# Optimization experiments

Measured on AMD Instinct MI355X. Metric: run time of the kernel, lower is better.

Reference implementation:

```python
import jax, jax.numpy as jnp
import numpy as np

NQ = 4   # num qubits
NL = 2   # StronglyEntanglingLayers depth


def _apply_1q(state, U, w):
    # state: (B,2,2,2,2) complex64, U: (2,2) complex64, wire w in [0,NQ)
    state = jnp.moveaxis(state, w + 1, -1)
    state = jnp.einsum('ij,...j->...i', U, state)
    return jnp.moveaxis(state, -1, w + 1)


def _apply_cnot(state, cw, tw):
    # flip target axis on the control=1 slice
    s0 = jnp.take(state, jnp.array([0]), axis=cw + 1)
    s1 = jnp.take(state, jnp.array([1]), axis=cw + 1)
    s1 = jnp.flip(s1, axis=tw + 1)
    return jnp.concatenate([s0, s1], axis=cw + 1)


def _simulate(xq, qw):
    # xq: (B, NQ) angles/pi, qw: (NL, NQ, 3) Rot params
    half = 0.5 * jnp.pi * xq                      # RY(pi*x) half-angles
    c, s = jnp.cos(half), jnp.sin(half)           # (B, NQ)
    # RY on |0> gives [cos(t/2), sin(t/2)]: build product state directly
    state = jnp.stack([c[:, 0], s[:, 0]], axis=-1).astype(jnp.complex64)  # (B,2)
    for w in range(1, NQ):
        q = jnp.stack([c[:, w], s[:, w]], axis=-1).astype(jnp.complex64)
        state = jnp.einsum('b...,bj->b...j', state, q)  # -> (B,2,...,2)

    for l in range(NL):
        for w in range(NQ):
            phi, theta, omega = qw[l, w, 0], qw[l, w, 1], qw[l, w, 2]
            ct = jnp.cos(0.5 * theta)
            st = jnp.sin(0.5 * theta)
            a = 0.5 * (phi + omega)
            b = 0.5 * (phi - omega)
            # PennyLane Rot(phi,theta,omega) = RZ(omega) RY(theta) RZ(phi)
            row0 = jnp.stack([jnp.exp(-1j * a) * ct, -jnp.exp(1j * b) * st])
            row1 = jnp.stack([jnp.exp(-1j * b) * st, jnp.exp(1j * a) * ct])
            U = jnp.stack([row0, row1]).astype(jnp.complex64)
            state = _apply_1q(state, U, w)
        r = l % (NQ - 1) + 1  # default ranges of StronglyEntanglingLayers
        for w in range(NQ):
            state = _apply_cnot(state, w, (w + r) % NQ)

    p = state.real ** 2 + state.imag ** 2  # (B,2,2,2,2) probabilities
    ez = []
    for w in range(NQ):
        axes = tuple(a for a in range(1, NQ + 1) if a != w + 1)
        m = p.sum(axis=axes)               # (B,2) marginal of wire w
        ez.append(m[:, 0] - m[:, 1])       # <PauliZ>
    return jnp.stack(ez, axis=1)           # (B, NQ) float32


def setup_inputs() -> dict:
    key = jax.random.key(0)
    ks = jax.random.split(key, 6)
    N, C, H, W, OUT = 8, 128, 128, 128, 128
    x = jax.random.normal(ks[0], (N, C, H, W), dtype=jnp.float32)
    pre_w = jax.random.normal(ks[1], (NQ, C), dtype=jnp.float32) * (1.0 / np.sqrt(C))
    pre_b = jax.random.normal(ks[2], (NQ,), dtype=jnp.float32) * 0.01
    q_weights = jax.random.normal(ks[3], (NL, NQ, 3), dtype=jnp.float32)
    post_w = jax.random.normal(ks[4], (OUT, NQ), dtype=jnp.float32) * 0.5
    post_b = jax.random.normal(ks[5], (OUT,), dtype=jnp.float32) * 0.01
    return {"x": x, "pre_w": pre_w, "pre_b": pre_b, "q_weights": q_weights,
            "post_w": post_w, "post_b": post_b}


def reference(x, pre_w, pre_b, q_weights, post_w, post_b):
    N, C, H, W = x.shape
    xf = x.transpose(0, 2, 3, 1).reshape(-1, C)      # (N*H*W, C)
    xq = xf @ pre_w.T + pre_b                        # (B, NQ)
    z = _simulate(xq, q_weights)                     # (B, NQ)
    out = z @ post_w.T + post_b                      # (B, OUT)
    return out.reshape(N, H, W, -1).transpose(0, 3, 1, 2)
```

## Files before the change

kernel.cpp:

```cpp
#include <hip/hip_runtime.h>
#include <math.h>

#define NQ   4
#define NL   2
#define CD   128
#define HWSZ 16384
#define OUTC 128

__global__ void qsetup_kernel(const float* __restrict__ qw, float* __restrict__ A) {
    __shared__ float Ur[16][17];
    __shared__ float Ui[16][17];
    __shared__ float sM[4 * 16 * 16];
    const int tid = threadIdx.x;

    if (tid < 16) {
        float sr[16], si[16];
        #pragma unroll
        for (int k = 0; k < 16; ++k) { sr[k] = (k == tid) ? 1.f : 0.f; si[k] = 0.f; }

        #pragma unroll
        for (int l = 0; l < NL; ++l) {
            #pragma unroll
            for (int w = 0; w < NQ; ++w) {
                float phi = qw[(l * NQ + w) * 3 + 0];
                float th  = qw[(l * NQ + w) * 3 + 1];
                float om  = qw[(l * NQ + w) * 3 + 2];
                float ct = cosf(0.5f * th), st = sinf(0.5f * th);
                float a = 0.5f * (phi + om), b = 0.5f * (phi - om);
                float sa, ca, sb, cb;
                sincosf(a, &sa, &ca);
                sincosf(b, &sb, &cb);
                float u00r =  ca * ct, u00i = -sa * ct;
                float u01r = -cb * st, u01i = -sb * st;
                float u10r =  cb * st, u10i = -sb * st;
                float u11r =  ca * ct, u11i =  sa * ct;
                const int wm = 1 << (3 - w);
                #pragma unroll
                for (int i = 0; i < 16; ++i) {
                    if (i & wm) continue;
                    int i1 = i | wm;
                    float a0r = sr[i],  a0i = si[i];
                    float a1r = sr[i1], a1i = si[i1];
                    sr[i]  = u00r * a0r - u00i * a0i + u01r * a1r - u01i * a1i;
                    si[i]  = u00r * a0i + u00i * a0r + u01r * a1i + u01i * a1r;
                    sr[i1] = u10r * a0r - u10i * a0i + u11r * a1r - u11i * a1i;
                    si[i1] = u10r * a0i + u10i * a0r + u11r * a1i + u11i * a1r;
                }
            }
            const int r = l % (NQ - 1) + 1;
            #pragma unroll
            for (int w = 0; w < NQ; ++w) {
                const int cm = 1 << (3 - w);
                const int tm = 1 << (3 - ((w + r) % NQ));
                #pragma unroll
                for (int i = 0; i < 16; ++i) {
                    if ((i & cm) && !(i & tm)) {
                        int i1 = i | tm;
                        float t;
                        t = sr[i]; sr[i] = sr[i1]; sr[i1] = t;
                        t = si[i]; si[i] = si[i1]; si[i1] = t;
                    }
                }
            }
        }
        #pragma unroll
        for (int k = 0; k < 16; ++k) { Ur[tid][k] = sr[k]; Ui[tid][k] = si[k]; }
    }
    __syncthreads();

    for (int t = tid; t < 4 * 16 * 16; t += blockDim.x) {
        int w = t >> 8, rem = t & 255, i = rem >> 4, j = rem & 15;
        float acc = 0.f;
        #pragma unroll
        for (int k = 0; k < 16; ++k) {
            float sgn = ((k >> (3 - w)) & 1) ? -1.f : 1.f;
            acc += sgn * (Ur[i][k] * Ur[j][k] + Ui[i][k] * Ui[j][k]);
        }
        sM[t] = acc;
    }
    __syncthreads();

    for (int t = tid; t < 4 * 81; t += blockDim.x) {
        int w = t / 81, j = t % 81;
        int j0 = j / 27, j1 = (j / 9) % 3, j2 = (j / 3) % 3, j3 = j % 3;
        int f =  ((j0 == 2) ? 8 : 0) | ((j1 == 2) ? 4 : 0)
               | ((j2 == 2) ? 2 : 0) | ((j3 == 2) ? 1 : 0);
        int zm = ((j0 == 1) ? 8 : 0) | ((j1 == 1) ? 4 : 0)
               | ((j2 == 1) ? 2 : 0) | ((j3 == 1) ? 1 : 0);
        float acc = 0.f;
        #pragma unroll
        for (int i = 0; i < 16; ++i) {
            float sgn = (__popc(i & zm) & 1) ? -1.f : 1.f;
            acc += sM[(w * 16 + (i ^ f)) * 16 + i] * sgn;
        }
        A[t] = acc * 0.0625f;
    }
}

__global__ __launch_bounds__(256) void qmain_kernel(
    const float* __restrict__ x, const float* __restrict__ pre_w,
    const float* __restrict__ pre_b, const float* __restrict__ A,
    const float* __restrict__ post_w, const float* __restrict__ post_b,
    float* __restrict__ out)
{
    const int tid = threadIdx.x;
    const int p  = blockIdx.x * 256 + tid;
    const int n  = p >> 14;
    const int hw = p & (HWSZ - 1);
    const float* xp = x + (size_t)n * CD * HWSZ + hw;

    float a0 = pre_b[0], a1 = pre_b[1], a2 = pre_b[2], a3 = pre_b[3];

    #pragma unroll
    for (int c0 = 0; c0 < CD; c0 += 32) {
        float xv[32];
        #pragma unroll
        for (int j = 0; j < 32; ++j)
            xv[j] = __builtin_nontemporal_load(&xp[(size_t)(c0 + j) * HWSZ]);
        #pragma unroll
        for (int j = 0; j < 32; ++j) {
            const int c = c0 + j;
            a0 = fmaf(xv[j], pre_w[0 * CD + c], a0);
            a1 = fmaf(xv[j], pre_w[1 * CD + c], a1);
            a2 = fmaf(xv[j], pre_w[2 * CD + c], a2);
            a3 = fmaf(xv[j], pre_w[3 * CD + c], a3);
        }
    }

    const float PI = 3.14159265358979323846f;
    float cz0, sx0, cz1, sx1, cz2, sx2, cz3, sx3;
    sincosf(PI * a0, &sx0, &cz0);
    sincosf(PI * a1, &sx1, &cz1);
    sincosf(PI * a2, &sx2, &cz2);
    sincosf(PI * a3, &sx3, &cz3);

    float g01[9], g23[9];
    {
        float t0[3] = { 1.f, cz0, sx0 }, t1[3] = { 1.f, cz1, sx1 };
        float t2[3] = { 1.f, cz2, sx2 }, t3[3] = { 1.f, cz3, sx3 };
        #pragma unroll
        for (int a = 0; a < 3; ++a)
            #pragma unroll
            for (int b = 0; b < 3; ++b) {
                g01[a * 3 + b] = t0[a] * t1[b];
                g23[a * 3 + b] = t2[a] * t3[b];
            }
    }

    float z0 = 0.f, z1 = 0.f, z2 = 0.f, z3 = 0.f;
    #pragma unroll
    for (int j01 = 0; j01 < 9; ++j01)
        #pragma unroll
        for (int j23 = 0; j23 < 9; ++j23) {
            float g = g01[j01] * g23[j23];
            int j = j01 * 9 + j23;
            z0 = fmaf(A[  0 + j], g, z0);
            z1 = fmaf(A[ 81 + j], g, z1);
            z2 = fmaf(A[162 + j], g, z2);
            z3 = fmaf(A[243 + j], g, z3);
        }

    float* op = out + (size_t)n * OUTC * HWSZ + hw;
    #pragma unroll 8
    for (int o = 0; o < OUTC; ++o) {
        float val = fmaf(z0, post_w[o * NQ + 0],
                    fmaf(z1, post_w[o * NQ + 1],
                    fmaf(z2, post_w[o * NQ + 2],
                    fmaf(z3, post_w[o * NQ + 3], post_b[o]))));
        __builtin_nontemporal_store(val, &op[(size_t)o * HWSZ]);
    }
}

extern "C" void kernel_launch(void* const* d_in, const int* in_sizes, int n_in,
                              void* d_out, int out_size, void* d_ws, size_t ws_size,
                              hipStream_t stream) {
    const float* x      = (const float*)d_in[0];
    const float* pre_w  = (const float*)d_in[1];
    const float* pre_b  = (const float*)d_in[2];
    const float* qw     = (const float*)d_in[3];
    const float* post_w = (const float*)d_in[4];
    const float* post_b = (const float*)d_in[5];
    float* out = (float*)d_out;
    float* A   = (float*)d_ws;

    hipLaunchKernelGGL(qsetup_kernel, dim3(1), dim3(256), 0, stream, qw, A);

    const int B = in_sizes[0] / CD;
    hipLaunchKernelGGL(qmain_kernel, dim3(B / 256), dim3(256), 0, stream,
                       x, pre_w, pre_b, A, post_w, post_b, out);
}
```

Baseline: 39.21 us.

## Split channel reduction and output channels across four wavefronts per pixel tile

```diff
diff --git a/kernel.cpp b/kernel.cpp
--- a/kernel.cpp
+++ b/kernel.cpp
@@ -6,6 +6,7 @@
 #define CD   128
 #define HWSZ 16384
 #define OUTC 128
+#define PIX  64
 
 __global__ void qsetup_kernel(const float* __restrict__ qw, float* __restrict__ A) {
     __shared__ float Ur[16][17];
@@ -103,28 +104,43 @@
     const float* __restrict__ post_w, const float* __restrict__ post_b,
     float* __restrict__ out)
 {
-    const int tid = threadIdx.x;
-    const int p  = blockIdx.x * 256 + tid;
-    const int n  = p >> 14;
-    const int hw = p & (HWSZ - 1);
-    const float* xp = x + (size_t)n * CD * HWSZ + hw;
+    __shared__ float part[4 * 4 * PIX];
+
+    const int tid    = threadIdx.x;
+    const int lane   = tid & 63;
+    const int q      = tid >> 6;
+    const int blk    = blockIdx.x;
+    const int n      = blk >> 8;
+    const int hwbase = (blk & 255) * PIX;
+    const float* xp  = x + (size_t)n * CD * HWSZ + hwbase + lane;
+
+    float xv[32];
+    #pragma unroll
+    for (int j = 0; j < 32; ++j)
+        xv[j] = __builtin_nontemporal_load(&xp[(size_t)(q * 32 + j) * HWSZ]);
+
+    float p0 = 0.f, p1 = 0.f, p2 = 0.f, p3 = 0.f;
+    #pragma unroll
+    for (int j = 0; j < 32; ++j) {
+        const int c = q * 32 + j;
+        p0 = fmaf(xv[j], pre_w[0 * CD + c], p0);
+        p1 = fmaf(xv[j], pre_w[1 * CD + c], p1);
+        p2 = fmaf(xv[j], pre_w[2 * CD + c], p2);
+        p3 = fmaf(xv[j], pre_w[3 * CD + c], p3);
+    }
+    part[(q * 4 + 0) * PIX + lane] = p0;
+    part[(q * 4 + 1) * PIX + lane] = p1;
+    part[(q * 4 + 2) * PIX + lane] = p2;
+    part[(q * 4 + 3) * PIX + lane] = p3;
+    __syncthreads();
 
     float a0 = pre_b[0], a1 = pre_b[1], a2 = pre_b[2], a3 = pre_b[3];
-
-    #pragma unroll
-    for (int c0 = 0; c0 < CD; c0 += 32) {
-        float xv[32];
-        #pragma unroll
-        for (int j = 0; j < 32; ++j)
-            xv[j] = __builtin_nontemporal_load(&xp[(size_t)(c0 + j) * HWSZ]);
-        #pragma unroll
-        for (int j = 0; j < 32; ++j) {
-            const int c = c0 + j;
-            a0 = fmaf(xv[j], pre_w[0 * CD + c], a0);
-            a1 = fmaf(xv[j], pre_w[1 * CD + c], a1);
-            a2 = fmaf(xv[j], pre_w[2 * CD + c], a2);
-            a3 = fmaf(xv[j], pre_w[3 * CD + c], a3);
-        }
+    #pragma unroll
+    for (int qq = 0; qq < 4; ++qq) {
+        a0 += part[(qq * 4 + 0) * PIX + lane];
+        a1 += part[(qq * 4 + 1) * PIX + lane];
+        a2 += part[(qq * 4 + 2) * PIX + lane];
+        a3 += part[(qq * 4 + 3) * PIX + lane];
     }
 
     const float PI = 3.14159265358979323846f;
@@ -160,9 +176,10 @@
             z3 = fmaf(A[243 + j], g, z3);
         }
 
-    float* op = out + (size_t)n * OUTC * HWSZ + hw;
+    float* op = out + (size_t)n * OUTC * HWSZ + hwbase + lane;
     #pragma unroll 8
-    for (int o = 0; o < OUTC; ++o) {
+    for (int i = 0; i < 32; ++i) {
+        const int o = q * 32 + i;
         float val = fmaf(z0, post_w[o * NQ + 0],
                     fmaf(z1, post_w[o * NQ + 1],
                     fmaf(z2, post_w[o * NQ + 2],
@@ -186,6 +203,6 @@
     hipLaunchKernelGGL(qsetup_kernel, dim3(1), dim3(256), 0, stream, qw, A);
 
     const int B = in_sizes[0] / CD;
-    hipLaunchKernelGGL(qmain_kernel, dim3(B / 256), dim3(256), 0, stream,
+    hipLaunchKernelGGL(qmain_kernel, dim3(B / PIX), dim3(256), 0, stream,
                        x, pre_w, pre_b, A, post_w, post_b, out);
 }
```

Result: slower. 53.64 us (+36.8%).

## Split projection/circuit and output expansion into separate kernels with vectorized stores

Applied to the files above, without the earlier changes.

```diff
diff --git a/kernel.cpp b/kernel.cpp
--- a/kernel.cpp
+++ b/kernel.cpp
@@ -6,6 +6,8 @@
 #define CD   128
 #define HWSZ 16384
 #define OUTC 128
+
+typedef float f4 __attribute__((ext_vector_type(4)));
 
 __global__ void qsetup_kernel(const float* __restrict__ qw, float* __restrict__ A) {
     __shared__ float Ur[16][17];
@@ -97,36 +99,10 @@
     }
 }
 
-__global__ __launch_bounds__(256) void qmain_kernel(
-    const float* __restrict__ x, const float* __restrict__ pre_w,
-    const float* __restrict__ pre_b, const float* __restrict__ A,
-    const float* __restrict__ post_w, const float* __restrict__ post_b,
-    float* __restrict__ out)
-{
-    const int tid = threadIdx.x;
-    const int p  = blockIdx.x * 256 + tid;
-    const int n  = p >> 14;
-    const int hw = p & (HWSZ - 1);
-    const float* xp = x + (size_t)n * CD * HWSZ + hw;
-
-    float a0 = pre_b[0], a1 = pre_b[1], a2 = pre_b[2], a3 = pre_b[3];
-
-    #pragma unroll
-    for (int c0 = 0; c0 < CD; c0 += 32) {
-        float xv[32];
-        #pragma unroll
-        for (int j = 0; j < 32; ++j)
-            xv[j] = __builtin_nontemporal_load(&xp[(size_t)(c0 + j) * HWSZ]);
-        #pragma unroll
-        for (int j = 0; j < 32; ++j) {
-            const int c = c0 + j;
-            a0 = fmaf(xv[j], pre_w[0 * CD + c], a0);
-            a1 = fmaf(xv[j], pre_w[1 * CD + c], a1);
-            a2 = fmaf(xv[j], pre_w[2 * CD + c], a2);
-            a3 = fmaf(xv[j], pre_w[3 * CD + c], a3);
-        }
-    }
-
+__device__ __forceinline__ void circuit_z(float a0, float a1, float a2, float a3,
+                                          const float* __restrict__ A,
+                                          float& z0, float& z1, float& z2, float& z3)
+{
     const float PI = 3.14159265358979323846f;
     float cz0, sx0, cz1, sx1, cz2, sx2, cz3, sx3;
     sincosf(PI * a0, &sx0, &cz0);
@@ -135,19 +111,17 @@
     sincosf(PI * a3, &sx3, &cz3);
 
     float g01[9], g23[9];
-    {
-        float t0[3] = { 1.f, cz0, sx0 }, t1[3] = { 1.f, cz1, sx1 };
-        float t2[3] = { 1.f, cz2, sx2 }, t3[3] = { 1.f, cz3, sx3 };
-        #pragma unroll
-        for (int a = 0; a < 3; ++a)
-            #pragma unroll
-            for (int b = 0; b < 3; ++b) {
-                g01[a * 3 + b] = t0[a] * t1[b];
-                g23[a * 3 + b] = t2[a] * t3[b];
-            }
-    }
-
-    float z0 = 0.f, z1 = 0.f, z2 = 0.f, z3 = 0.f;
+    float t0[3] = { 1.f, cz0, sx0 }, t1[3] = { 1.f, cz1, sx1 };
+    float t2[3] = { 1.f, cz2, sx2 }, t3[3] = { 1.f, cz3, sx3 };
+    #pragma unroll
+    for (int a = 0; a < 3; ++a)
+        #pragma unroll
+        for (int b = 0; b < 3; ++b) {
+            g01[a * 3 + b] = t0[a] * t1[b];
+            g23[a * 3 + b] = t2[a] * t3[b];
+        }
+
+    z0 = z1 = z2 = z3 = 0.f;
     #pragma unroll
     for (int j01 = 0; j01 < 9; ++j01)
         #pragma unroll
@@ -159,6 +133,104 @@
             z2 = fmaf(A[162 + j], g, z2);
             z3 = fmaf(A[243 + j], g, z3);
         }
+}
+
+__global__ __launch_bounds__(64, 4) void dotz_kernel(
+    const float* __restrict__ x, const float* __restrict__ pre_w,
+    const float* __restrict__ pre_b, const float* __restrict__ A,
+    f4* __restrict__ zbuf)
+{
+    const int lane = threadIdx.x;
+    const int b    = blockIdx.x;
+    const int p    = b * 64 + lane;
+    const int n    = p >> 14;
+    const int hw   = p & (HWSZ - 1);
+    const float* xp = x + (size_t)n * CD * HWSZ + hw;
+
+    float a0 = pre_b[0], a1 = pre_b[1], a2 = pre_b[2], a3 = pre_b[3];
+    #pragma unroll
+    for (int c0 = 0; c0 < CD; c0 += 32) {
+        float xv[32];
+        #pragma unroll
+        for (int j = 0; j < 32; ++j)
+            xv[j] = xp[(size_t)(c0 + j) * HWSZ];
+        #pragma unroll
+        for (int j = 0; j < 32; ++j) {
+            const int c = c0 + j;
+            a0 = fmaf(xv[j], pre_w[0 * CD + c], a0);
+            a1 = fmaf(xv[j], pre_w[1 * CD + c], a1);
+            a2 = fmaf(xv[j], pre_w[2 * CD + c], a2);
+            a3 = fmaf(xv[j], pre_w[3 * CD + c], a3);
+        }
+    }
+
+    float z0, z1, z2, z3;
+    circuit_z(a0, a1, a2, a3, A, z0, z1, z2, z3);
+    f4 zv; zv.x = z0; zv.y = z1; zv.z = z2; zv.w = z3;
+    zbuf[p] = zv;
+}
+
+__global__ __launch_bounds__(64, 4) void expand_kernel(
+    const f4* __restrict__ zbuf, const float* __restrict__ post_w,
+    const float* __restrict__ post_b, float* __restrict__ out)
+{
+    const int lane  = threadIdx.x;
+    const int b     = blockIdx.x;
+    const int chunk = b & 63;
+    const int n     = (b >> 6) & 7;
+    const int oq    = b >> 9;
+
+    const int pqi = chunk * 64 + lane;
+    const int hw0 = pqi * 4;
+    const f4* zp = zbuf + (size_t)n * HWSZ + hw0;
+    f4 za = zp[0], zb = zp[1], zc = zp[2], zd = zp[3];
+
+    float* op = out + (size_t)n * OUTC * HWSZ + hw0;
+    #pragma unroll 8
+    for (int i = 0; i < 32; ++i) {
+        const int o = oq * 32 + i;
+        const f4 wv = *reinterpret_cast<const f4*>(&post_w[o * NQ]);
+        const float bias = post_b[o];
+        f4 v;
+        v.x = fmaf(za.x, wv.x, fmaf(za.y, wv.y, fmaf(za.z, wv.z, fmaf(za.w, wv.w, bias))));
+        v.y = fmaf(zb.x, wv.x, fmaf(zb.y, wv.y, fmaf(zb.z, wv.z, fmaf(zb.w, wv.w, bias))));
+        v.z = fmaf(zc.x, wv.x, fmaf(zc.y, wv.y, fmaf(zc.z, wv.z, fmaf(zc.w, wv.w, bias))));
+        v.w = fmaf(zd.x, wv.x, fmaf(zd.y, wv.y, fmaf(zd.z, wv.z, fmaf(zd.w, wv.w, bias))));
+        __builtin_nontemporal_store(v, reinterpret_cast<f4*>(&op[(size_t)o * HWSZ]));
+    }
+}
+
+__global__ __launch_bounds__(256) void qmain_kernel(
+    const float* __restrict__ x, const float* __restrict__ pre_w,
+    const float* __restrict__ pre_b, const float* __restrict__ A,
+    const float* __restrict__ post_w, const float* __restrict__ post_b,
+    float* __restrict__ out)
+{
+    const int tid = threadIdx.x;
+    const int p  = blockIdx.x * 256 + tid;
+    const int n  = p >> 14;
+    const int hw = p & (HWSZ - 1);
+    const float* xp = x + (size_t)n * CD * HWSZ + hw;
+
+    float a0 = pre_b[0], a1 = pre_b[1], a2 = pre_b[2], a3 = pre_b[3];
+    #pragma unroll
+    for (int c0 = 0; c0 < CD; c0 += 32) {
+        float xv[32];
+        #pragma unroll
+        for (int j = 0; j < 32; ++j)
+            xv[j] = xp[(size_t)(c0 + j) * HWSZ];
+        #pragma unroll
+        for (int j = 0; j < 32; ++j) {
+            const int c = c0 + j;
+            a0 = fmaf(xv[j], pre_w[0 * CD + c], a0);
+            a1 = fmaf(xv[j], pre_w[1 * CD + c], a1);
+            a2 = fmaf(xv[j], pre_w[2 * CD + c], a2);
+            a3 = fmaf(xv[j], pre_w[3 * CD + c], a3);
+        }
+    }
+
+    float z0, z1, z2, z3;
+    circuit_z(a0, a1, a2, a3, A, z0, z1, z2, z3);
 
     float* op = out + (size_t)n * OUTC * HWSZ + hw;
     #pragma unroll 8
@@ -181,11 +253,23 @@
     const float* post_w = (const float*)d_in[4];
     const float* post_b = (const float*)d_in[5];
     float* out = (float*)d_out;
-    float* A   = (float*)d_ws;
+
+    float* A = (float*)d_ws;
+    const size_t z_off   = 2048;
+    const size_t z_bytes = (size_t)(8 * HWSZ) * 4 * sizeof(float);
 
     hipLaunchKernelGGL(qsetup_kernel, dim3(1), dim3(256), 0, stream, qw, A);
 
     const int B = in_sizes[0] / CD;
-    hipLaunchKernelGGL(qmain_kernel, dim3(B / 256), dim3(256), 0, stream,
-                       x, pre_w, pre_b, A, post_w, post_b, out);
-}
+
+    if (ws_size >= z_off + z_bytes) {
+        f4* zbuf = (f4*)((char*)d_ws + z_off);
+        hipLaunchKernelGGL(dotz_kernel, dim3(B / 64), dim3(64), 0, stream,
+                           x, pre_w, pre_b, A, zbuf);
+        hipLaunchKernelGGL(expand_kernel, dim3(B / 64), dim3(64), 0, stream,
+                           zbuf, post_w, post_b, out);
+    } else {
+        hipLaunchKernelGGL(qmain_kernel, dim3(B / 256), dim3(256), 0, stream,
+                           x, pre_w, pre_b, A, post_w, post_b, out);
+    }
+}
```

After: 54.29 us. 1.38x slower.

## Process four pixels per thread with float4 vectorized loads and stores

Applied to the files above, without the earlier changes.

```diff
diff --git a/kernel.cpp b/kernel.cpp
--- a/kernel.cpp
+++ b/kernel.cpp
@@ -6,6 +6,8 @@
 #define CD   128
 #define HWSZ 16384
 #define OUTC 128
+
+typedef float f4 __attribute__((ext_vector_type(4)));
 
 __global__ void qsetup_kernel(const float* __restrict__ qw, float* __restrict__ A) {
     __shared__ float Ur[16][17];
@@ -97,36 +99,10 @@
     }
 }
 
-__global__ __launch_bounds__(256) void qmain_kernel(
-    const float* __restrict__ x, const float* __restrict__ pre_w,
-    const float* __restrict__ pre_b, const float* __restrict__ A,
-    const float* __restrict__ post_w, const float* __restrict__ post_b,
-    float* __restrict__ out)
+__device__ __forceinline__ void circuit_z(float a0, float a1, float a2, float a3,
+                                          const float* __restrict__ A,
+                                          float& z0, float& z1, float& z2, float& z3)
 {
-    const int tid = threadIdx.x;
-    const int p  = blockIdx.x * 256 + tid;
-    const int n  = p >> 14;
-    const int hw = p & (HWSZ - 1);
-    const float* xp = x + (size_t)n * CD * HWSZ + hw;
-
-    float a0 = pre_b[0], a1 = pre_b[1], a2 = pre_b[2], a3 = pre_b[3];
-
-    #pragma unroll
-    for (int c0 = 0; c0 < CD; c0 += 32) {
-        float xv[32];
-        #pragma unroll
-        for (int j = 0; j < 32; ++j)
-            xv[j] = __builtin_nontemporal_load(&xp[(size_t)(c0 + j) * HWSZ]);
-        #pragma unroll
-        for (int j = 0; j < 32; ++j) {
-            const int c = c0 + j;
-            a0 = fmaf(xv[j], pre_w[0 * CD + c], a0);
-            a1 = fmaf(xv[j], pre_w[1 * CD + c], a1);
-            a2 = fmaf(xv[j], pre_w[2 * CD + c], a2);
-            a3 = fmaf(xv[j], pre_w[3 * CD + c], a3);
-        }
-    }
-
     const float PI = 3.14159265358979323846f;
     float cz0, sx0, cz1, sx1, cz2, sx2, cz3, sx3;
     sincosf(PI * a0, &sx0, &cz0);
@@ -135,19 +111,17 @@
     sincosf(PI * a3, &sx3, &cz3);
 
     float g01[9], g23[9];
-    {
-        float t0[3] = { 1.f, cz0, sx0 }, t1[3] = { 1.f, cz1, sx1 };
-        float t2[3] = { 1.f, cz2, sx2 }, t3[3] = { 1.f, cz3, sx3 };
-        #pragma unroll
-        for (int a = 0; a < 3; ++a)
-            #pragma unroll
-            for (int b = 0; b < 3; ++b) {
-                g01[a * 3 + b] = t0[a] * t1[b];
-                g23[a * 3 + b] = t2[a] * t3[b];
-            }
-    }
-
-    float z0 = 0.f, z1 = 0.f, z2 = 0.f, z3 = 0.f;
+    float t0[3] = { 1.f, cz0, sx0 }, t1[3] = { 1.f, cz1, sx1 };
+    float t2[3] = { 1.f, cz2, sx2 }, t3[3] = { 1.f, cz3, sx3 };
+    #pragma unroll
+    for (int a = 0; a < 3; ++a)
+        #pragma unroll
+        for (int b = 0; b < 3; ++b) {
+            g01[a * 3 + b] = t0[a] * t1[b];
+            g23[a * 3 + b] = t2[a] * t3[b];
+        }
+
+    z0 = z1 = z2 = z3 = 0.f;
     #pragma unroll
     for (int j01 = 0; j01 < 9; ++j01)
         #pragma unroll
@@ -159,15 +133,66 @@
             z2 = fmaf(A[162 + j], g, z2);
             z3 = fmaf(A[243 + j], g, z3);
         }
-
-    float* op = out + (size_t)n * OUTC * HWSZ + hw;
+}
+
+__global__ __launch_bounds__(64) void qquad_kernel(
+    const float* __restrict__ x, const float* __restrict__ pre_w,
+    const float* __restrict__ pre_b, const float* __restrict__ A,
+    const float* __restrict__ post_w, const float* __restrict__ post_b,
+    float* __restrict__ out)
+{
+    const int lane = threadIdx.x;
+    const int pq   = blockIdx.x * 64 + lane;
+    const int n    = pq >> 12;
+    const int hw0  = (pq & 4095) * 4;
+    const float* xp = x + (size_t)n * CD * HWSZ + hw0;
+
+    float acc[4][4];
+    #pragma unroll
+    for (int px = 0; px < 4; ++px)
+        #pragma unroll
+        for (int q = 0; q < 4; ++q)
+            acc[px][q] = pre_b[q];
+
+    #pragma unroll
+    for (int c0 = 0; c0 < CD; c0 += 16) {
+        f4 xv[16];
+        #pragma unroll
+        for (int j = 0; j < 16; ++j)
+            xv[j] = *reinterpret_cast<const f4*>(&xp[(size_t)(c0 + j) * HWSZ]);
+        #pragma unroll
+        for (int j = 0; j < 16; ++j) {
+            const int c = c0 + j;
+            const float w0 = pre_w[0 * CD + c], w1 = pre_w[1 * CD + c];
+            const float w2 = pre_w[2 * CD + c], w3 = pre_w[3 * CD + c];
+            #pragma unroll
+            for (int px = 0; px < 4; ++px) {
+                const float xs = xv[j][px];
+                acc[px][0] = fmaf(xs, w0, acc[px][0]);
+                acc[px][1] = fmaf(xs, w1, acc[px][1]);
+                acc[px][2] = fmaf(xs, w2, acc[px][2]);
+                acc[px][3] = fmaf(xs, w3, acc[px][3]);
+            }
+        }
+    }
+
+    float z[4][4];
+    #pragma unroll
+    for (int px = 0; px < 4; ++px)
+        circuit_z(acc[px][0], acc[px][1], acc[px][2], acc[px][3], A,
+                  z[px][0], z[px][1], z[px][2], z[px][3]);
+
+    float* op = out + (size_t)n * OUTC * HWSZ + hw0;
     #pragma unroll 8
     for (int o = 0; o < OUTC; ++o) {
-        float val = fmaf(z0, post_w[o * NQ + 0],
-                    fmaf(z1, post_w[o * NQ + 1],
-                    fmaf(z2, post_w[o * NQ + 2],
-                    fmaf(z3, post_w[o * NQ + 3], post_b[o]))));
-        __builtin_nontemporal_store(val, &op[(size_t)o * HWSZ]);
+        const f4 wv = *reinterpret_cast<const f4*>(&post_w[o * NQ]);
+        const float bias = post_b[o];
+        f4 v;
+        #pragma unroll
+        for (int px = 0; px < 4; ++px)
+            v[px] = fmaf(z[px][0], wv.x, fmaf(z[px][1], wv.y,
+                    fmaf(z[px][2], wv.z, fmaf(z[px][3], wv.w, bias))));
+        __builtin_nontemporal_store(v, reinterpret_cast<f4*>(&op[(size_t)o * HWSZ]));
     }
 }
 
@@ -186,6 +211,6 @@
     hipLaunchKernelGGL(qsetup_kernel, dim3(1), dim3(256), 0, stream, qw, A);
 
     const int B = in_sizes[0] / CD;
-    hipLaunchKernelGGL(qmain_kernel, dim3(B / 256), dim3(256), 0, stream,
+    hipLaunchKernelGGL(qquad_kernel, dim3(B / 4 / 64), dim3(64), 0, stream,
                        x, pre_w, pre_b, A, post_w, post_b, out);
 }
```

New measurement: 91.72 us. 2.34x slower.
